# Optimization experiments

Measured on AMD Instinct MI355X. Metric: run time of the kernel, lower is better.

## Reference

```python
import jax, jax.numpy as jnp
import numpy as np

N, E, C, R = 50000, 800000, 64, 8
H = 64  # MLP hidden width


def setup_inputs() -> dict:
    key = jax.random.key(0)
    ks = jax.random.split(key, 11)
    return {
        "node_features": jax.random.normal(ks[0], (N, 4 * C), jnp.float32),  # [0e: C] ++ [1o: C*3]
        "sph_harmonics": jax.random.normal(ks[1], (E, 4), jnp.float32),      # [Y_00, Y_1m (3)]
        "radial_basis": jax.random.normal(ks[2], (E, R), jnp.float32),
        "pre_W0": jax.random.normal(ks[3], (C, C), jnp.float32),
        "pre_W1": jax.random.normal(ks[4], (C, C), jnp.float32),
        "mlp_W1": jax.random.normal(ks[5], (R, H), jnp.float32) / np.sqrt(R),
        "mlp_W2": jax.random.normal(ks[6], (H, H), jnp.float32) / np.sqrt(H),
        "mlp_W3": jax.random.normal(ks[7], (H, 4 * C), jnp.float32) / np.sqrt(H),
        "post_W0": jax.random.normal(ks[8], (C, C), jnp.float32),
        "post_W1": jax.random.normal(ks[9], (C, C), jnp.float32),
        "edge_index": jax.random.randint(ks[10], (2, E), 0, N),  # row 0: receiver, row 1: sender
    }


def reference(node_features, sph_harmonics, radial_basis,
              pre_W0, pre_W1, mlp_W1, mlp_W2, mlp_W3, post_W0, post_W1,
              edge_index):
    n = node_features.shape[0]
    c = pre_W0.shape[0]
    inv_sqrt_c = 1.0 / jnp.sqrt(jnp.asarray(c, jnp.float32))
    INV_SQRT2 = 0.7071067811865476   # path normalization (2 paths per output irrep)
    INV_SQRT3 = 0.5773502691896258   # CG norm for 1o x 1o -> 0e (dot)

    # split flattened irreps: scalars [n, c], vectors [n, c, 3]
    x0 = node_features[:, :c]
    x1 = node_features[:, c:].reshape(n, c, 3)

    # pre_linear: per-irrep channel mixing (e3nn o3.Linear with 1/sqrt(fan_in))
    x0 = (x0 @ pre_W0) * inv_sqrt_c
    x1 = jnp.einsum('ncm,cd->ndm', x1, pre_W1) * inv_sqrt_c

    recv, send = edge_index[0], edge_index[1]

    # gather neighbour features (irregular access)
    xj0 = x0[send]            # [E, c]
    xj1 = x1[send]            # [E, c, 3]
    sh0 = sph_harmonics[:, :1]  # [E, 1]
    sh1 = sph_harmonics[:, 1:]  # [E, 3]

    # per-edge generated tensor-product weights: SiLU MLP, no bias, linear last layer
    h = jax.nn.silu(radial_basis @ mlp_W1)
    h = jax.nn.silu(h @ mlp_W2)
    w = h @ mlp_W3            # [E, 4c]
    w00, w110, w01, w10 = w[:, :c], w[:, c:2 * c], w[:, 2 * c:3 * c], w[:, 3 * c:]

    # channelwise CG tensor product with per-edge weights
    # 0e outputs: (0e x 0e) and (1o . 1o)/sqrt(3)
    m0 = (w00 * xj0 * sh0 + w110 * (jnp.einsum('ecm,em->ec', xj1, sh1) * INV_SQRT3)) * INV_SQRT2
    # 1o outputs: (0e x 1o) and (1o x 0e)
    m1 = (w01[:, :, None] * xj0[:, :, None] * sh1[:, None, :]
          + w10[:, :, None] * xj1 * sh0[:, :, None]) * INV_SQRT2   # [E, c, 3]

    # scatter-reduce (sum aggregation) into receiving nodes
    agg0 = jax.ops.segment_sum(m0, recv, num_segments=n)           # [n, c]
    agg1 = jax.ops.segment_sum(m1, recv, num_segments=n)           # [n, c, 3]

    # post_linear: per-irrep channel mixing
    y0 = (agg0 @ post_W0) * inv_sqrt_c
    y1 = jnp.einsum('ncm,cd->ndm', agg1, post_W1) * inv_sqrt_c

    # UnflattenIrreps -> [n, channels, sum(2l+1)] = [n, c, 4]
    return jnp.concatenate([y0[:, :, None], y1], axis=-1)
```

## Files before the change

kernel.cpp:

```cpp
#include <hip/hip_runtime.h>


#define FDIM 256
#define INV_SQRT2 0.7071067811865476f
#define INV_SQRT3 0.5773502691896258f

typedef __attribute__((ext_vector_type(8))) short s16x8;
typedef __attribute__((ext_vector_type(4))) float fx4;

__device__ __forceinline__ float silu_f(float x) { return x / (1.0f + __expf(-x)); }

__device__ __forceinline__ unsigned short f2bf(float x) {
    unsigned int u = __float_as_uint(x);
    u += 0x7FFFu + ((u >> 16) & 1u);
    return (unsigned short)(u >> 16);
}

__device__ __forceinline__ float bf2f(short v) {
    return __uint_as_float(((unsigned int)(unsigned short)v) << 16);
}

__device__ __forceinline__ int swz(int row) {
    return ((row & 7) ^ ((row >> 3) & 7)) << 4;
}

__global__ void __launch_bounds__(256) hist_kernel(
    const int* __restrict__ ei, int* __restrict__ cnt, int E,
    const float* __restrict__ W1, const float* __restrict__ W2,
    const float* __restrict__ W3, float* __restrict__ W1t,
    unsigned short* __restrict__ W2bf, unsigned short* __restrict__ W3bf)
{
    int i = blockIdx.x * 256 + threadIdx.x;
    if (i < 512)  { int r = i >> 6, k = i & 63; W1t[k * 8 + r] = W1[i]; }
    if (i < 4096) { int j = i >> 6, k = i & 63; W2bf[i] = f2bf(W2[k * 64 + j]); }
    if (i < 16384) {
        int col = i >> 6, k = i & 63;
        int cb = col >> 5, r32 = col & 31, t = r32 >> 3, ci = r32 & 7;
        W3bf[i] = f2bf(W3[k * 256 + t * 64 + cb * 8 + ci]);
    }
    if (i < E) atomicAdd(&cnt[ei[i]], 1);
}

__global__ void __launch_bounds__(1024) scan_kernel(
    const int* __restrict__ cnt, int* __restrict__ cursor, int nBins)
{
    __shared__ int part[1024];
    const int t = threadIdx.x;
    const int per = (nBins + 1023) / 1024;
    const int lo = t * per;
    const int hi = (lo + per < nBins) ? lo + per : nBins;

    int s = 0;
    for (int i = lo; i < hi; ++i) s += cnt[i];
    part[t] = s;
    __syncthreads();

    for (int off = 1; off < 1024; off <<= 1) {
        int v = part[t];
        int add = (t >= off) ? part[t - off] : 0;
        __syncthreads();
        part[t] = v + add;
        __syncthreads();
    }

    int run = part[t] - s;
    for (int i = lo; i < hi; ++i) {
        cursor[i] = run;
        run += cnt[i];
    }
}

__global__ void __launch_bounds__(256) scatter_perm_kernel(
    const int* __restrict__ ei, int* __restrict__ cursor,
    int* __restrict__ perm, int2* __restrict__ ers, int E)
{
    int i = blockIdx.x * 256 + threadIdx.x;
    if (i < E) {
        int r = ei[i];
        int p = atomicAdd(&cursor[r], 1);
        perm[p] = i;
        ers[p] = make_int2(r, ei[E + i]);
    }
}

__global__ void __launch_bounds__(256) pre_kernel(
    const float* __restrict__ nf, const float* __restrict__ W0,
    const float* __restrict__ W1, unsigned short* __restrict__ xtb, int nNodes)
{
    const int lane = threadIdx.x & 63;
    const int wave = threadIdx.x >> 6;
    const int waveId = blockIdx.x * 4 + wave;
    const int nWaves = gridDim.x * 4;

    __shared__ __align__(16) float rowL[4][256];

    float w0r[64], w1r[64];
#pragma unroll
    for (int c = 0; c < 64; ++c) {
        w0r[c] = W0[c * 64 + lane];
        w1r[c] = W1[c * 64 + lane];
    }

    for (int n = waveId; n < nNodes; n += nWaves) {
        float4 rv = *reinterpret_cast<const float4*>(nf + (size_t)n * FDIM + lane * 4);
        *reinterpret_cast<float4*>(&rowL[wave][lane * 4]) = rv;
        asm volatile("s_waitcnt lgkmcnt(0)" ::: "memory");
        __builtin_amdgcn_sched_barrier(0);

        float a0 = 0.f, a1 = 0.f, a2 = 0.f, a3 = 0.f;
#pragma unroll
        for (int c4 = 0; c4 < 16; ++c4) {
            fx4 x0 = *reinterpret_cast<const fx4*>(&rowL[wave][c4 * 4]);
            fx4 xa = *reinterpret_cast<const fx4*>(&rowL[wave][64 + c4 * 12]);
            fx4 xb = *reinterpret_cast<const fx4*>(&rowL[wave][64 + c4 * 12 + 4]);
            fx4 xc = *reinterpret_cast<const fx4*>(&rowL[wave][64 + c4 * 12 + 8]);
            const int c = c4 * 4;
            a0 = fmaf(x0[0], w0r[c + 0], a0);
            a1 = fmaf(xa[0], w1r[c + 0], a1);
            a2 = fmaf(xa[1], w1r[c + 0], a2);
            a3 = fmaf(xa[2], w1r[c + 0], a3);
            a0 = fmaf(x0[1], w0r[c + 1], a0);
            a1 = fmaf(xa[3], w1r[c + 1], a1);
            a2 = fmaf(xb[0], w1r[c + 1], a2);
            a3 = fmaf(xb[1], w1r[c + 1], a3);
            a0 = fmaf(x0[2], w0r[c + 2], a0);
            a1 = fmaf(xb[2], w1r[c + 2], a1);
            a2 = fmaf(xb[3], w1r[c + 2], a2);
            a3 = fmaf(xc[0], w1r[c + 2], a3);
            a0 = fmaf(x0[3], w0r[c + 3], a0);
            a1 = fmaf(xc[1], w1r[c + 3], a1);
            a2 = fmaf(xc[2], w1r[c + 3], a2);
            a3 = fmaf(xc[3], w1r[c + 3], a3);
        }
        __builtin_amdgcn_sched_barrier(0);

        unsigned short* o = xtb + (size_t)n * FDIM + (lane >> 3) * 32 + (lane & 7);
        o[0]  = f2bf(a0 * 0.125f);
        o[8]  = f2bf(a1 * 0.125f);
        o[16] = f2bf(a2 * 0.125f);
        o[24] = f2bf(a3 * 0.125f);
    }
}

__global__ void __launch_bounds__(256, 2) edge_kernel(
    const unsigned short* __restrict__ xtb, const float* __restrict__ sph,
    const float* __restrict__ rb, const int2* __restrict__ ers,
    const int* __restrict__ perm,
    const float* __restrict__ W1t, const unsigned short* __restrict__ W2bf,
    const unsigned short* __restrict__ W3bf, float* __restrict__ agg, int E)
{
    const int tid  = threadIdx.x;
    const int lane = tid & 63;
    const int wave = tid >> 6;
    const int eBase = blockIdx.x * 256 + wave * 64;
    const int idx = eBase + lane;
    const int idxSafe = (idx < E) ? idx : (E - 1);
    const int pe = perm[idxSafe];

    __shared__ __align__(16) char sbufAll[4][16384];
    __shared__ int recvL[4][64];
    char* const sbuf = sbufAll[wave];

    const float4 rq0 = *reinterpret_cast<const float4*>(rb + (size_t)pe * 8);
    const float4 rq1 = *reinterpret_cast<const float4*>(rb + (size_t)pe * 8 + 4);
    const float rbv[8] = {rq0.x, rq0.y, rq0.z, rq0.w, rq1.x, rq1.y, rq1.z, rq1.w};

    float h1[64];
#pragma unroll
    for (int k = 0; k < 64; ++k) {
        float acc = 0.f;
#pragma unroll
        for (int r = 0; r < 8; ++r) acc = fmaf(rbv[r], W1t[k * 8 + r], acc);
        h1[k] = silu_f(acc);
    }

#pragma unroll
    for (int q = 0; q < 8; ++q) {
        s16x8 v;
#pragma unroll
        for (int t = 0; t < 8; ++t) v[t] = (short)f2bf(h1[q * 8 + t]);
        *reinterpret_cast<s16x8*>(sbuf + lane * 128 + ((q * 16) ^ swz(lane))) = v;
    }

    const float4 shv = *reinterpret_cast<const float4*>(sph + (size_t)pe * 4);
    const float sh1a[3] = {shv.y, shv.z, shv.w};
    const int2 rs = ers[idxSafe];
    recvL[wave][lane] = rs.x;
    const unsigned short* __restrict__ xrow = xtb + (size_t)rs.y * FDIM;

    const int l15 = lane & 15;
    const int g4  = lane >> 4;

    s16x8 aH[4][2];
#pragma unroll
    for (int m = 0; m < 4; ++m)
#pragma unroll
        for (int kk = 0; kk < 2; ++kk) {
            int row = m * 16 + l15;
            aH[m][kk] = *reinterpret_cast<const s16x8*>(
                sbuf + row * 128 + ((kk * 64 + g4 * 16) ^ swz(row)));
        }

#pragma unroll
    for (int nh = 0; nh < 2; ++nh) {
        s16x8 bW2[2][2];
#pragma unroll
        for (int n2 = 0; n2 < 2; ++n2)
#pragma unroll
            for (int kk = 0; kk < 2; ++kk)
                bW2[n2][kk] = *reinterpret_cast<const s16x8*>(
                    W2bf + ((nh * 2 + n2) * 16 + l15) * 64 + kk * 32 + g4 * 8);

        fx4 acc2[4][2];
#pragma unroll
        for (int m = 0; m < 4; ++m)
#pragma unroll
            for (int n2 = 0; n2 < 2; ++n2) {
                fx4 z = {0.f, 0.f, 0.f, 0.f};
                acc2[m][n2] = z;
            }
#pragma unroll
        for (int kk = 0; kk < 2; ++kk)
#pragma unroll
            for (int m = 0; m < 4; ++m)
#pragma unroll
                for (int n2 = 0; n2 < 2; ++n2)
                    acc2[m][n2] = __builtin_amdgcn_mfma_f32_16x16x32_bf16(
                        aH[m][kk], bW2[n2][kk], acc2[m][n2], 0, 0, 0);

#pragma unroll
        for (int m = 0; m < 4; ++m)
#pragma unroll
            for (int n2 = 0; n2 < 2; ++n2)
#pragma unroll
                for (int r = 0; r < 4; ++r) {
                    int edge = m * 16 + g4 * 4 + r;
                    int j = (nh * 2 + n2) * 16 + l15;
                    *reinterpret_cast<unsigned short*>(
                        sbuf + edge * 128 + ((2 * j) ^ swz(edge))) =
                        f2bf(silu_f(acc2[m][n2][r]));
                }
    }

    s16x8 aH2[4][2];
#pragma unroll
    for (int m = 0; m < 4; ++m)
#pragma unroll
        for (int kk = 0; kk < 2; ++kk) {
            int row = m * 16 + l15;
            aH2[m][kk] = *reinterpret_cast<const s16x8*>(
                sbuf + row * 128 + ((kk * 64 + g4 * 16) ^ swz(row)));
        }

    const int jj  = lane & 31;
    const int sub = lane >> 5;
    const int base = sub * 32;
    float* const aggJJ = agg + jj;

    unsigned segmask = 0;
    {
        int rp = recvL[wave][base];
#pragma unroll
        for (int ep = 1; ep < 32; ++ep) {
            int r = recvL[wave][base + ep];
            if (r != rp) segmask |= (1u << ep);
            rp = r;
        }
    }

    for (int cbp = 0; cbp < 4; ++cbp) {
        s16x8 xjb2[8];
#pragma unroll
        for (int t = 0; t < 8; ++t)
            xjb2[t] = *reinterpret_cast<const s16x8*>(xrow + cbp * 64 + t * 8);

#pragma unroll
        for (int half = 0; half < 2; ++half) {
            const int cb = cbp * 2 + half;
            const s16x8* xjb = &xjb2[half * 4];

            s16x8 bW3[2][2];
#pragma unroll
            for (int n2 = 0; n2 < 2; ++n2)
#pragma unroll
                for (int kk = 0; kk < 2; ++kk)
                    bW3[n2][kk] = *reinterpret_cast<const s16x8*>(
                        W3bf + (cb * 32 + n2 * 16 + l15) * 64 + kk * 32 + g4 * 8);

            fx4 accw[4][2];
#pragma unroll
            for (int m = 0; m < 4; ++m)
#pragma unroll
                for (int n2 = 0; n2 < 2; ++n2) {
                    fx4 z = {0.f, 0.f, 0.f, 0.f};
                    accw[m][n2] = z;
                }
#pragma unroll
            for (int kk = 0; kk < 2; ++kk)
#pragma unroll
                for (int m = 0; m < 4; ++m)
#pragma unroll
                    for (int n2 = 0; n2 < 2; ++n2)
                        accw[m][n2] = __builtin_amdgcn_mfma_f32_16x16x32_bf16(
                            aH2[m][kk], bW3[n2][kk], accw[m][n2], 0, 0, 0);

#pragma unroll
            for (int m = 0; m < 4; ++m)
#pragma unroll
                for (int n2 = 0; n2 < 2; ++n2)
#pragma unroll
                    for (int r = 0; r < 4; ++r) {
                        int edge = m * 16 + g4 * 4 + r;
                        int c32 = n2 * 16 + l15;
                        *reinterpret_cast<float*>(
                            sbuf + edge * 128 + ((c32 * 4) ^ swz(edge))) = accw[m][n2][r];
                    }

            float wv[4][8];
#pragma unroll
            for (int t = 0; t < 4; ++t)
#pragma unroll
                for (int q = 0; q < 2; ++q) {
                    fx4 v = *reinterpret_cast<const fx4*>(
                        sbuf + lane * 128 + ((t * 32 + q * 16) ^ swz(lane)));
                    wv[t][q*4+0]=v.x; wv[t][q*4+1]=v.y; wv[t][q*4+2]=v.z; wv[t][q*4+3]=v.w;
                }

#pragma unroll
            for (int ci = 0; ci < 8; ++ci) {
                float x0v = bf2f(xjb[0][ci]);
                float x1a = bf2f(xjb[1][ci]);
                float x1b = bf2f(xjb[2][ci]);
                float x1c = bf2f(xjb[3][ci]);
                float dotv = (x1a * sh1a[0] + x1b * sh1a[1] + x1c * sh1a[2]) * INV_SQRT3;
                float m0 = (wv[0][ci] * x0v * shv.x + wv[1][ci] * dotv) * INV_SQRT2;
                float m1 = (wv[2][ci] * x0v * sh1a[0] + wv[3][ci] * x1a * shv.x) * INV_SQRT2;
                float m2 = (wv[2][ci] * x0v * sh1a[1] + wv[3][ci] * x1b * shv.x) * INV_SQRT2;
                float m3 = (wv[2][ci] * x0v * sh1a[2] + wv[3][ci] * x1c * shv.x) * INV_SQRT2;
                wv[0][ci] = m0; wv[1][ci] = m1; wv[2][ci] = m2; wv[3][ci] = m3;
            }
#pragma unroll
            for (int t = 0; t < 4; ++t)
#pragma unroll
                for (int q = 0; q < 2; ++q) {
                    fx4 v = {wv[t][q*4+0], wv[t][q*4+1], wv[t][q*4+2], wv[t][q*4+3]};
                    *reinterpret_cast<fx4*>(
                        sbuf + lane * 128 + ((t * 32 + q * 16) ^ swz(lane))) = v;
                }

            {
                int rprev = recvL[wave][base];
                float acc = 0.f;
                bool first = true;
#pragma unroll
                for (int ep = 0; ep < 32; ++ep) {
                    const int eL = base + ep;
                    float v = *reinterpret_cast<const float*>(
                        sbuf + eL * 128 + ((jj * 4) ^ swz(eL)));
                    if (eBase + eL >= E) v = 0.f;
                    if (segmask & (1u << ep)) {
                        float* dst = aggJJ + (size_t)rprev * FDIM + cb * 32;
                        if (first) atomicAdd(dst, acc);
                        else       *dst = acc;
                        first = false;
                        acc = 0.f;
                        rprev = recvL[wave][eL];
                    }
                    acc += v;
                }
                atomicAdd(aggJJ + (size_t)rprev * FDIM + cb * 32, acc);
            }
        }
    }
}

__global__ void __launch_bounds__(256) post_kernel(
    const float* __restrict__ agg, const float* __restrict__ W0,
    const float* __restrict__ W1, float* __restrict__ out, int nNodes)
{
    const int lane = threadIdx.x & 63;
    const int wave = threadIdx.x >> 6;
    const int waveId = blockIdx.x * 4 + wave;
    const int nWaves = gridDim.x * 4;

    __shared__ __align__(16) float rowL[4][256];

    float w0r[64], w1r[64];
#pragma unroll
    for (int c = 0; c < 64; ++c) {
        w0r[c] = W0[c * 64 + lane];
        w1r[c] = W1[c * 64 + lane];
    }

    for (int n = waveId; n < nNodes; n += nWaves) {
        float4 rv = *reinterpret_cast<const float4*>(agg + (size_t)n * FDIM + lane * 4);
        *reinterpret_cast<float4*>(&rowL[wave][lane * 4]) = rv;
        asm volatile("s_waitcnt lgkmcnt(0)" ::: "memory");
        __builtin_amdgcn_sched_barrier(0);

        float a0 = 0.f, a1 = 0.f, a2 = 0.f, a3 = 0.f;
#pragma unroll
        for (int cb = 0; cb < 8; ++cb)
#pragma unroll
            for (int q = 0; q < 2; ++q) {
                const int c = cb * 8 + q * 4;
                fx4 v0 = *reinterpret_cast<const fx4*>(&rowL[wave][cb*32 + q*4]);
                fx4 v1 = *reinterpret_cast<const fx4*>(&rowL[wave][cb*32 + 8 + q*4]);
                fx4 v2 = *reinterpret_cast<const fx4*>(&rowL[wave][cb*32 + 16 + q*4]);
                fx4 v3 = *reinterpret_cast<const fx4*>(&rowL[wave][cb*32 + 24 + q*4]);
#pragma unroll
                for (int j = 0; j < 4; ++j) {
                    a0 = fmaf(v0[j], w0r[c + j], a0);
                    a1 = fmaf(v1[j], w1r[c + j], a1);
                    a2 = fmaf(v2[j], w1r[c + j], a2);
                    a3 = fmaf(v3[j], w1r[c + j], a3);
                }
            }
        __builtin_amdgcn_sched_barrier(0);

        float4 o4;
        o4.x = a0 * 0.125f;
        o4.y = a1 * 0.125f;
        o4.z = a2 * 0.125f;
        o4.w = a3 * 0.125f;
        *reinterpret_cast<float4*>(out + (size_t)n * FDIM + lane * 4) = o4;
    }
}

extern "C" void kernel_launch(void* const* d_in, const int* in_sizes, int n_in,
                              void* d_out, int out_size, void* d_ws, size_t ws_size,
                              hipStream_t stream) {
    const float* nf     = (const float*)d_in[0];
    const float* sph    = (const float*)d_in[1];
    const float* rb     = (const float*)d_in[2];
    const float* preW0  = (const float*)d_in[3];
    const float* preW1  = (const float*)d_in[4];
    const float* mlpW1  = (const float*)d_in[5];
    const float* mlpW2  = (const float*)d_in[6];
    const float* mlpW3  = (const float*)d_in[7];
    const float* postW0 = (const float*)d_in[8];
    const float* postW1 = (const float*)d_in[9];
    const int*   ei     = (const int*)d_in[10];

    const int N = in_sizes[0] / FDIM;
    const int E = in_sizes[1] / 4;

    float* agg = (float*)d_ws;
    unsigned short* xtb = (unsigned short*)(agg + (size_t)N * FDIM);
    float* W1t = (float*)(xtb + (size_t)N * FDIM);
    unsigned short* W2bf = (unsigned short*)(W1t + 512);
    unsigned short* W3bf = W2bf + 4096;
    int* cnt    = (int*)(W3bf + 16384);
    int* cursor = cnt + N;
    int* perm   = cursor + N;
    int2* ers   = (int2*)(perm + E);

    hipMemsetAsync(agg, 0, (size_t)N * FDIM * sizeof(float), stream);
    hipMemsetAsync(cnt, 0, (size_t)N * sizeof(int), stream);

    hist_kernel<<<(E + 255) / 256, 256, 0, stream>>>(
        ei, cnt, E, mlpW1, mlpW2, mlpW3, W1t, W2bf, W3bf);
    pre_kernel<<<2048, 256, 0, stream>>>(nf, preW0, preW1, xtb, N);
    scan_kernel<<<1, 1024, 0, stream>>>(cnt, cursor, N);
    scatter_perm_kernel<<<(E + 255) / 256, 256, 0, stream>>>(ei, cursor, perm, ers, E);
    edge_kernel<<<(E + 255) / 256, 256, 0, stream>>>(
        xtb, sph, rb, ers, perm, W1t, W2bf, W3bf, agg, E);
    post_kernel<<<2048, 256, 0, stream>>>(agg, postW0, postW1, (float*)d_out, N);
}
```

Before: 514.6 us.

## Fuse histogram with pre-linear, double-buffer node rows, merge memsets

Merges the edge histogram and weight-preparation kernel with the pre-linear node transform into one launch. The pre and post node loops now prefetch the next node row into a second LDS buffer while computing the current one. The count array is placed right after the aggregation buffer so a single memset clears both. The goals are fewer launches and hiding global-load latency in the node loops. The cost is that the fused kernel runs with the E/256 grid and every thread loads 128 weight registers, which may hurt occupancy for the histogram part.

```diff
diff --git a/kernel.cpp b/kernel.cpp
--- a/kernel.cpp
+++ b/kernel.cpp
@@ -24,11 +24,14 @@
     return ((row & 7) ^ ((row >> 3) & 7)) << 4;
 }
 
-__global__ void __launch_bounds__(256) hist_kernel(
+__global__ void __launch_bounds__(256) hist_pre_kernel(
     const int* __restrict__ ei, int* __restrict__ cnt, int E,
     const float* __restrict__ W1, const float* __restrict__ W2,
     const float* __restrict__ W3, float* __restrict__ W1t,
-    unsigned short* __restrict__ W2bf, unsigned short* __restrict__ W3bf)
+    unsigned short* __restrict__ W2bf, unsigned short* __restrict__ W3bf,
+    const float* __restrict__ nf, const float* __restrict__ preW0,
+    const float* __restrict__ preW1, unsigned short* __restrict__ xtb,
+    int nNodes)
 {
     int i = blockIdx.x * 256 + threadIdx.x;
     if (i < 512)  { int r = i >> 6, k = i & 63; W1t[k * 8 + r] = W1[i]; }
@@ -39,81 +42,45 @@
         W3bf[i] = f2bf(W3[k * 256 + t * 64 + cb * 8 + ci]);
     }
     if (i < E) atomicAdd(&cnt[ei[i]], 1);
-}
-
-__global__ void __launch_bounds__(1024) scan_kernel(
-    const int* __restrict__ cnt, int* __restrict__ cursor, int nBins)
-{
-    __shared__ int part[1024];
-    const int t = threadIdx.x;
-    const int per = (nBins + 1023) / 1024;
-    const int lo = t * per;
-    const int hi = (lo + per < nBins) ? lo + per : nBins;
-
-    int s = 0;
-    for (int i = lo; i < hi; ++i) s += cnt[i];
-    part[t] = s;
-    __syncthreads();
-
-    for (int off = 1; off < 1024; off <<= 1) {
-        int v = part[t];
-        int add = (t >= off) ? part[t - off] : 0;
-        __syncthreads();
-        part[t] = v + add;
-        __syncthreads();
-    }
-
-    int run = part[t] - s;
-    for (int i = lo; i < hi; ++i) {
-        cursor[i] = run;
-        run += cnt[i];
-    }
-}
-
-__global__ void __launch_bounds__(256) scatter_perm_kernel(
-    const int* __restrict__ ei, int* __restrict__ cursor,
-    int* __restrict__ perm, int2* __restrict__ ers, int E)
-{
-    int i = blockIdx.x * 256 + threadIdx.x;
-    if (i < E) {
-        int r = ei[i];
-        int p = atomicAdd(&cursor[r], 1);
-        perm[p] = i;
-        ers[p] = make_int2(r, ei[E + i]);
-    }
-}
-
-__global__ void __launch_bounds__(256) pre_kernel(
-    const float* __restrict__ nf, const float* __restrict__ W0,
-    const float* __restrict__ W1, unsigned short* __restrict__ xtb, int nNodes)
-{
+
     const int lane = threadIdx.x & 63;
     const int wave = threadIdx.x >> 6;
     const int waveId = blockIdx.x * 4 + wave;
     const int nWaves = gridDim.x * 4;
 
-    __shared__ __align__(16) float rowL[4][256];
+    __shared__ __align__(16) float rowL[4][2][256];
 
     float w0r[64], w1r[64];
 #pragma unroll
     for (int c = 0; c < 64; ++c) {
-        w0r[c] = W0[c * 64 + lane];
-        w1r[c] = W1[c * 64 + lane];
-    }
-
-    for (int n = waveId; n < nNodes; n += nWaves) {
+        w0r[c] = preW0[c * 64 + lane];
+        w1r[c] = preW1[c * 64 + lane];
+    }
+
+    int n = waveId;
+    if (n < nNodes) {
         float4 rv = *reinterpret_cast<const float4*>(nf + (size_t)n * FDIM + lane * 4);
-        *reinterpret_cast<float4*>(&rowL[wave][lane * 4]) = rv;
+        *reinterpret_cast<float4*>(&rowL[wave][0][lane * 4]) = rv;
+    }
+    int buf = 0;
+    for (; n < nNodes; n += nWaves, buf ^= 1) {
+        const int nn = n + nWaves;
+        const bool hasNext = (nn < nNodes);
+        float4 rvn;
+        if (hasNext)
+            rvn = *reinterpret_cast<const float4*>(nf + (size_t)nn * FDIM + lane * 4);
+
         asm volatile("s_waitcnt lgkmcnt(0)" ::: "memory");
         __builtin_amdgcn_sched_barrier(0);
 
+        const float* __restrict__ row = rowL[wave][buf];
         float a0 = 0.f, a1 = 0.f, a2 = 0.f, a3 = 0.f;
 #pragma unroll
         for (int c4 = 0; c4 < 16; ++c4) {
-            fx4 x0 = *reinterpret_cast<const fx4*>(&rowL[wave][c4 * 4]);
-            fx4 xa = *reinterpret_cast<const fx4*>(&rowL[wave][64 + c4 * 12]);
-            fx4 xb = *reinterpret_cast<const fx4*>(&rowL[wave][64 + c4 * 12 + 4]);
-            fx4 xc = *reinterpret_cast<const fx4*>(&rowL[wave][64 + c4 * 12 + 8]);
+            fx4 x0 = *reinterpret_cast<const fx4*>(&row[c4 * 4]);
+            fx4 xa = *reinterpret_cast<const fx4*>(&row[64 + c4 * 12]);
+            fx4 xb = *reinterpret_cast<const fx4*>(&row[64 + c4 * 12 + 4]);
+            fx4 xc = *reinterpret_cast<const fx4*>(&row[64 + c4 * 12 + 8]);
             const int c = c4 * 4;
             a0 = fmaf(x0[0], w0r[c + 0], a0);
             a1 = fmaf(xa[0], w1r[c + 0], a1);
@@ -139,6 +106,52 @@
         o[8]  = f2bf(a1 * 0.125f);
         o[16] = f2bf(a2 * 0.125f);
         o[24] = f2bf(a3 * 0.125f);
+
+        if (hasNext)
+            *reinterpret_cast<float4*>(&rowL[wave][buf ^ 1][lane * 4]) = rvn;
+        __builtin_amdgcn_sched_barrier(0);
+    }
+}
+
+__global__ void __launch_bounds__(1024) scan_kernel(
+    const int* __restrict__ cnt, int* __restrict__ cursor, int nBins)
+{
+    __shared__ int part[1024];
+    const int t = threadIdx.x;
+    const int per = (nBins + 1023) / 1024;
+    const int lo = t * per;
+    const int hi = (lo + per < nBins) ? lo + per : nBins;
+
+    int s = 0;
+    for (int i = lo; i < hi; ++i) s += cnt[i];
+    part[t] = s;
+    __syncthreads();
+
+    for (int off = 1; off < 1024; off <<= 1) {
+        int v = part[t];
+        int add = (t >= off) ? part[t - off] : 0;
+        __syncthreads();
+        part[t] = v + add;
+        __syncthreads();
+    }
+
+    int run = part[t] - s;
+    for (int i = lo; i < hi; ++i) {
+        cursor[i] = run;
+        run += cnt[i];
+    }
+}
+
+__global__ void __launch_bounds__(256) scatter_perm_kernel(
+    const int* __restrict__ ei, int* __restrict__ cursor,
+    int* __restrict__ perm, int2* __restrict__ ers, int E)
+{
+    int i = blockIdx.x * 256 + threadIdx.x;
+    if (i < E) {
+        int r = ei[i];
+        int p = atomicAdd(&cursor[r], 1);
+        perm[p] = i;
+        ers[p] = make_int2(r, ei[E + i]);
     }
 }
 
@@ -383,7 +396,7 @@
     const int waveId = blockIdx.x * 4 + wave;
     const int nWaves = gridDim.x * 4;
 
-    __shared__ __align__(16) float rowL[4][256];
+    __shared__ __align__(16) float rowL[4][2][256];
 
     float w0r[64], w1r[64];
 #pragma unroll
@@ -392,22 +405,33 @@
         w1r[c] = W1[c * 64 + lane];
     }
 
-    for (int n = waveId; n < nNodes; n += nWaves) {
+    int n = waveId;
+    if (n < nNodes) {
         float4 rv = *reinterpret_cast<const float4*>(agg + (size_t)n * FDIM + lane * 4);
-        *reinterpret_cast<float4*>(&rowL[wave][lane * 4]) = rv;
+        *reinterpret_cast<float4*>(&rowL[wave][0][lane * 4]) = rv;
+    }
+    int buf = 0;
+    for (; n < nNodes; n += nWaves, buf ^= 1) {
+        const int nn = n + nWaves;
+        const bool hasNext = (nn < nNodes);
+        float4 rvn;
+        if (hasNext)
+            rvn = *reinterpret_cast<const float4*>(agg + (size_t)nn * FDIM + lane * 4);
+
         asm volatile("s_waitcnt lgkmcnt(0)" ::: "memory");
         __builtin_amdgcn_sched_barrier(0);
 
+        const float* __restrict__ row = rowL[wave][buf];
         float a0 = 0.f, a1 = 0.f, a2 = 0.f, a3 = 0.f;
 #pragma unroll
         for (int cb = 0; cb < 8; ++cb)
 #pragma unroll
             for (int q = 0; q < 2; ++q) {
                 const int c = cb * 8 + q * 4;
-                fx4 v0 = *reinterpret_cast<const fx4*>(&rowL[wave][cb*32 + q*4]);
-                fx4 v1 = *reinterpret_cast<const fx4*>(&rowL[wave][cb*32 + 8 + q*4]);
-                fx4 v2 = *reinterpret_cast<const fx4*>(&rowL[wave][cb*32 + 16 + q*4]);
-                fx4 v3 = *reinterpret_cast<const fx4*>(&rowL[wave][cb*32 + 24 + q*4]);
+                fx4 v0 = *reinterpret_cast<const fx4*>(&row[cb*32 + q*4]);
+                fx4 v1 = *reinterpret_cast<const fx4*>(&row[cb*32 + 8 + q*4]);
+                fx4 v2 = *reinterpret_cast<const fx4*>(&row[cb*32 + 16 + q*4]);
+                fx4 v3 = *reinterpret_cast<const fx4*>(&row[cb*32 + 24 + q*4]);
 #pragma unroll
                 for (int j = 0; j < 4; ++j) {
                     a0 = fmaf(v0[j], w0r[c + j], a0);
@@ -424,6 +448,10 @@
         o4.z = a2 * 0.125f;
         o4.w = a3 * 0.125f;
         *reinterpret_cast<float4*>(out + (size_t)n * FDIM + lane * 4) = o4;
+
+        if (hasNext)
+            *reinterpret_cast<float4*>(&rowL[wave][buf ^ 1][lane * 4]) = rvn;
+        __builtin_amdgcn_sched_barrier(0);
     }
 }
 
@@ -446,21 +474,21 @@
     const int E = in_sizes[1] / 4;
 
     float* agg = (float*)d_ws;
-    unsigned short* xtb = (unsigned short*)(agg + (size_t)N * FDIM);
+    int* cnt = (int*)(agg + (size_t)N * FDIM);
+    unsigned short* xtb = (unsigned short*)(cnt + N);
     float* W1t = (float*)(xtb + (size_t)N * FDIM);
     unsigned short* W2bf = (unsigned short*)(W1t + 512);
     unsigned short* W3bf = W2bf + 4096;
-    int* cnt    = (int*)(W3bf + 16384);
-    int* cursor = cnt + N;
+    int* cursor = (int*)(W3bf + 16384);
     int* perm   = cursor + N;
     int2* ers   = (int2*)(perm + E);
 
-    hipMemsetAsync(agg, 0, (size_t)N * FDIM * sizeof(float), stream);
-    hipMemsetAsync(cnt, 0, (size_t)N * sizeof(int), stream);
-
-    hist_kernel<<<(E + 255) / 256, 256, 0, stream>>>(
-        ei, cnt, E, mlpW1, mlpW2, mlpW3, W1t, W2bf, W3bf);
-    pre_kernel<<<2048, 256, 0, stream>>>(nf, preW0, preW1, xtb, N);
+    hipMemsetAsync(agg, 0, (size_t)N * FDIM * sizeof(float) + (size_t)N * sizeof(int),
+                   stream);
+
+    hist_pre_kernel<<<(E + 255) / 256, 256, 0, stream>>>(
+        ei, cnt, E, mlpW1, mlpW2, mlpW3, W1t, W2bf, W3bf,
+        nf, preW0, preW1, xtb, N);
     scan_kernel<<<1, 1024, 0, stream>>>(cnt, cursor, N);
     scatter_perm_kernel<<<(E + 255) / 256, 256, 0, stream>>>(ei, cursor, perm, ers, E);
     edge_kernel<<<(E + 255) / 256, 256, 0, stream>>>(
```

Result: faster. 490.6 us (-4.7%).
